# Optimization experiments

Hardware: AMD Instinct MI355X
Metric: run time of the kernel (lower is better)

## Reference

```python
import jax, jax.numpy as jnp
import numpy as np

N = 50000
IN_F = 256
HID = 32
HEADS = 4
NEG_SLOPE = 0.2


def _gat_layer(x, edge_index, W, a_src, a_dst, bias):
    # x: [N, Fin]; W: [Fin, H*C]; a_src/a_dst: [H, C]; bias: [H*C]
    n = x.shape[0]
    H, C = a_src.shape
    h = (x @ W).reshape(n, H, C)                     # [N, H, C]
    alpha_src = jnp.einsum('nhc,hc->nh', h, a_src)   # [N, H]
    alpha_dst = jnp.einsum('nhc,hc->nh', h, a_dst)   # [N, H]
    src, dst = edge_index[0], edge_index[1]
    logits = alpha_src[src] + alpha_dst[dst]         # [E, H]
    logits = jax.nn.leaky_relu(logits, negative_slope=NEG_SLOPE)
    # segment softmax over edges grouped by destination node
    seg_max = jax.ops.segment_max(logits, dst, num_segments=n)
    seg_max = jnp.where(jnp.isfinite(seg_max), seg_max, 0.0)
    e = jnp.exp(logits - seg_max[dst])               # [E, H]
    denom = jax.ops.segment_sum(e, dst, num_segments=n)  # [N, H]
    attn = e / (denom[dst] + 1e-16)                  # [E, H]
    msg = h[src] * attn[:, :, None]                  # [E, H, C]
    out = jax.ops.segment_sum(msg, dst, num_segments=n)  # [N, H, C]
    return out.reshape(n, H * C) + bias


def _add_self_loops(edge_index, n):
    # PyG GATConv default add_self_loops=True
    loops = jnp.arange(n, dtype=edge_index.dtype)
    return jnp.concatenate([edge_index, jnp.stack([loops, loops])], axis=1)


def setup_inputs() -> dict:
    key = jax.random.key(0)
    ks = jax.random.split(key, 10)
    x = jax.random.normal(ks[0], (N, IN_F), dtype=jnp.float32)
    edge_index = jax.random.randint(ks[1], (2, 800000), 0, N, dtype=jnp.int64)
    d1 = HEADS * HID
    s1 = 1.0 / np.sqrt(IN_F)
    W1 = jax.random.normal(ks[2], (IN_F, d1), dtype=jnp.float32) * s1
    a_src1 = jax.random.normal(ks[3], (HEADS, HID), dtype=jnp.float32) * 0.1
    a_dst1 = jax.random.normal(ks[4], (HEADS, HID), dtype=jnp.float32) * 0.1
    b1 = jnp.zeros((d1,), dtype=jnp.float32)
    s2 = 1.0 / np.sqrt(d1)
    W2 = jax.random.normal(ks[5], (d1, d1), dtype=jnp.float32) * s2
    a_src2 = jax.random.normal(ks[6], (HEADS, HID), dtype=jnp.float32) * 0.1
    a_dst2 = jax.random.normal(ks[7], (HEADS, HID), dtype=jnp.float32) * 0.1
    b2 = jnp.zeros((d1,), dtype=jnp.float32)
    return {"x": x, "edge_index": edge_index, "W1": W1, "a_src1": a_src1,
            "a_dst1": a_dst1, "b1": b1, "W2": W2, "a_src2": a_src2,
            "a_dst2": a_dst2, "b2": b2}


def reference(x, edge_index, W1, a_src1, a_dst1, b1, W2, a_src2, a_dst2, b2):
    # Inference mode: dropout layers are identity.
    ei = _add_self_loops(edge_index, x.shape[0])
    h = _gat_layer(x, ei, W1, a_src1, a_dst1, b1)
    h = jax.nn.elu(h)
    h = _gat_layer(h, ei, W2, a_src2, a_dst2, b2)
    return h
```

## Files before the change

### kernel.cpp

```cpp
#include <hip/hip_runtime.h>
#include <hip/hip_fp16.h>
#include <math.h>

#define HEADS 4
#define HID 32
#define D1 128
#define IN_FEAT 256
#define NEG_SLOPE 0.2f
#define CAP 64
#define AGG_NODES 4
#define NPASS 8

#define WTS_STRIDE_H 72
#define HTS_STRIDE_H 136
#define SMEM_BYTES (128 * 272)

typedef _Float16 half8 __attribute__((ext_vector_type(8)));
typedef float f32x4 __attribute__((ext_vector_type(4)));
typedef long long ll2 __attribute__((ext_vector_type(2)));

static inline int ceil_div(int a, int b) { return (a + b - 1) / b; }

static __device__ inline float2 unpack_h2(unsigned int v) {
    __half2 h = __builtin_bit_cast(__half2, v);
    return __half22float2(h);
}

__global__ void init_prep(const unsigned int* __restrict__ raw, int* __restrict__ flag,
                          const float* __restrict__ W1, _Float16* __restrict__ WT1,
                          const float* __restrict__ W2, _Float16* __restrict__ WT2) {
    int i = blockIdx.x * blockDim.x + threadIdx.x;
    if (i < IN_FEAT * D1) {
        int k = i >> 7, n = i & 127;
        WT1[(size_t)n * IN_FEAT + k] = (_Float16)W1[i];
    }
    if (i < D1 * D1) {
        int k = i >> 7, n = i & 127;
        WT2[(size_t)n * D1 + k] = (_Float16)W2[i];
    }
    if (blockIdx.x == 0 && threadIdx.x < 64) {
        unsigned int hi = raw[2 * threadIdx.x + 1];
        unsigned long long b = __ballot(hi != 0u);
        if (threadIdx.x == 0) *flag = (b == 0ULL) ? 1 : 0;
    }
}

__global__ __launch_bounds__(256) void scatter_slots(const void* __restrict__ raw,
                                                     const int* __restrict__ flag,
                                                     int* __restrict__ cnt,
                                                     unsigned short* __restrict__ slots,
                                                     int E, int N) {
    const int e0 = (blockIdx.x * blockDim.x + threadIdx.x) * 4;
    const bool wide = (*flag != 0);
    int s[4], d[4];
    bool val[4];
    if (e0 + 4 <= E) {
        if (wide) {
            const ll2* ps = (const ll2*)((const long long*)raw + e0);
            const ll2* pd = (const ll2*)((const long long*)raw + E + e0);
            ll2 a = ps[0], b = ps[1], c = pd[0], e = pd[1];
            s[0] = (int)a[0]; s[1] = (int)a[1]; s[2] = (int)b[0]; s[3] = (int)b[1];
            d[0] = (int)c[0]; d[1] = (int)c[1]; d[2] = (int)e[0]; d[3] = (int)e[1];
        } else {
            int4 a = *(const int4*)((const int*)raw + e0);
            int4 b = *(const int4*)((const int*)raw + E + e0);
            s[0] = a.x; s[1] = a.y; s[2] = a.z; s[3] = a.w;
            d[0] = b.x; d[1] = b.y; d[2] = b.z; d[3] = b.w;
        }
        val[0] = val[1] = val[2] = val[3] = true;
    } else {
#pragma unroll
        for (int i = 0; i < 4; ++i) {
            int e = e0 + i;
            val[i] = (e < E);
            if (val[i]) {
                if (wide) { s[i] = (int)((const long long*)raw)[e]; d[i] = (int)((const long long*)raw)[E + e]; }
                else      { s[i] = ((const int*)raw)[e];            d[i] = ((const int*)raw)[E + e]; }
            } else { s[i] = 0; d[i] = 0; }
        }
    }

    const int range = (N + NPASS - 1) / NPASS;
    int lo = 0;
    for (int p = 0; p < NPASS; ++p, lo += range) {
        const int hi = lo + range;
#pragma unroll
        for (int i = 0; i < 4; ++i) {
            if (val[i] && d[i] >= lo && d[i] < hi) {
                int pos = atomicAdd(&cnt[d[i]], 1);
                if (pos < CAP) slots[(size_t)d[i] * CAP + pos] = (unsigned short)s[i];
            }
        }
        __syncthreads();
    }
}

template <int AF16>
__global__ __launch_bounds__(256) void gemm128(const void* __restrict__ Ain,
                                               const _Float16* __restrict__ WT,
                                               _Float16* __restrict__ Hout,
                                               const float* __restrict__ a_src,
                                               const float* __restrict__ a_dst,
                                               float* __restrict__ asrc_out,
                                               float* __restrict__ adst_out,
                                               int M, int K) {
    __shared__ __align__(16) char smem[SMEM_BYTES];
    _Float16* WTs = (_Float16*)smem;

    const int tid = threadIdx.x;
    const int wave = tid >> 6, lane = tid & 63;
    const int quad = lane >> 4, l16 = lane & 15;
    const int row0 = blockIdx.x * 128;
    const int m0 = min(row0 + wave * 32 + l16, M - 1);
    const int m1 = min(row0 + wave * 32 + 16 + l16, M - 1);
    const float*    Af = (const float*)Ain;
    const _Float16* Ah = (const _Float16*)Ain;
    const uint4* WTg = (const uint4*)WT;
    const int K8 = K >> 3;

    f32x4 acc[2][8];
#pragma unroll
    for (int r = 0; r < 2; ++r)
#pragma unroll
        for (int c = 0; c < 8; ++c) acc[r][c] = (f32x4){0.f, 0.f, 0.f, 0.f};

    for (int kb = 0; kb < K; kb += 64) {
        __syncthreads();
#pragma unroll
        for (int i = 0; i < 4; ++i) {
            int c = tid + i * 256;
            int n = c >> 3, j = c & 7;
            uint4 v = WTg[(size_t)n * K8 + (kb >> 3) + j];
            *(uint4*)(smem + n * 144 + j * 16) = v;
        }
        __syncthreads();
#pragma unroll
        for (int kc = 0; kc < 2; ++kc) {
            int k0 = kb + kc * 32 + quad * 8;
            half8 a0f, a1f;
            if (AF16) {
                a0f = *(const half8*)(Ah + (size_t)m0 * K + k0);
                a1f = *(const half8*)(Ah + (size_t)m1 * K + k0);
            } else {
                float4 x0 = *(const float4*)(Af + (size_t)m0 * K + k0);
                float4 x1 = *(const float4*)(Af + (size_t)m0 * K + k0 + 4);
                float4 y0 = *(const float4*)(Af + (size_t)m1 * K + k0);
                float4 y1 = *(const float4*)(Af + (size_t)m1 * K + k0 + 4);
                a0f[0] = (_Float16)x0.x; a0f[1] = (_Float16)x0.y;
                a0f[2] = (_Float16)x0.z; a0f[3] = (_Float16)x0.w;
                a0f[4] = (_Float16)x1.x; a0f[5] = (_Float16)x1.y;
                a0f[6] = (_Float16)x1.z; a0f[7] = (_Float16)x1.w;
                a1f[0] = (_Float16)y0.x; a1f[1] = (_Float16)y0.y;
                a1f[2] = (_Float16)y0.z; a1f[3] = (_Float16)y0.w;
                a1f[4] = (_Float16)y1.x; a1f[5] = (_Float16)y1.y;
                a1f[6] = (_Float16)y1.z; a1f[7] = (_Float16)y1.w;
            }
#pragma unroll
            for (int c = 0; c < 8; ++c) {
                half8 bf = *(const half8*)(smem + (c * 16 + l16) * 144 + kc * 64 + quad * 16);
                acc[0][c] = __builtin_amdgcn_mfma_f32_16x16x32_f16(a0f, bf, acc[0][c], 0, 0, 0);
                acc[1][c] = __builtin_amdgcn_mfma_f32_16x16x32_f16(a1f, bf, acc[1][c], 0, 0, 0);
            }
        }
    }

    __syncthreads();
    _Float16* hts = (_Float16*)smem;
#pragma unroll
    for (int r = 0; r < 2; ++r)
#pragma unroll
        for (int c = 0; c < 8; ++c)
#pragma unroll
            for (int g = 0; g < 4; ++g) {
                int row = wave * 32 + r * 16 + quad * 4 + g;
                hts[row * HTS_STRIDE_H + c * 16 + l16] = (_Float16)acc[r][c][g];
            }
    __syncthreads();

    const int r = tid >> 1;
    const int part = tid & 1;
    const int grow = row0 + r;
    const uint4* hrow = (const uint4*)(smem + r * 272 + part * 128);
    if (grow < M) {
        uint4* dv = (uint4*)(Hout + (size_t)grow * 128 + part * 64);
#pragma unroll
        for (int i = 0; i < 8; ++i) dv[i] = hrow[i];
    }
#pragma unroll
    for (int t = 0; t < 2; ++t) {
        int hh = part * 2 + t;
        const uint4* hv = (const uint4*)(smem + r * 272 + hh * 64);
        const float4* as4 = (const float4*)(a_src + hh * HID);
        const float4* ad4 = (const float4*)(a_dst + hh * HID);
        float ps = 0.f, pd = 0.f;
#pragma unroll
        for (int b = 0; b < 4; ++b) {
            uint4 u = hv[b];
            float2 f0 = unpack_h2(u.x), f1 = unpack_h2(u.y);
            float2 f2 = unpack_h2(u.z), f3 = unpack_h2(u.w);
            float4 s0 = as4[b * 2], s1 = as4[b * 2 + 1];
            float4 d0 = ad4[b * 2], d1 = ad4[b * 2 + 1];
            ps += f0.x * s0.x + f0.y * s0.y + f1.x * s0.z + f1.y * s0.w
                + f2.x * s1.x + f2.y * s1.y + f3.x * s1.z + f3.y * s1.w;
            pd += f0.x * d0.x + f0.y * d0.y + f1.x * d0.z + f1.y * d0.w
                + f2.x * d1.x + f2.y * d1.y + f3.x * d1.z + f3.y * d1.w;
        }
        if (grow < M) {
            asrc_out[grow * 4 + hh] = ps;
            adst_out[grow * 4 + hh] = pd;
        }
    }
}

__global__ __launch_bounds__(256) void aggregate(const _Float16* __restrict__ hb,
                                                 const int* __restrict__ cnt,
                                                 const unsigned short* __restrict__ slots,
                                                 const float* __restrict__ asrc,
                                                 const float* __restrict__ adst,
                                                 const float* __restrict__ bias,
                                                 float* __restrict__ out32,
                                                 _Float16* __restrict__ out16,
                                                 int N, int apply_elu) {
    const int w = threadIdx.x >> 6;
    const int lane = threadIdx.x & 63;
    const int node = blockIdx.x * AGG_NODES + w;
    const bool live = (node < N);

    __shared__ float wsh[AGG_NODES][CAP][4];
    __shared__ int ssh[AGG_NODES][CAP];

    int cntE = 0, count = 1;
    if (live) {
        cntE = min(cnt[node], CAP - 1);
        count = cntE + 1;
    }
    const unsigned short* nslots = slots + (size_t)node * CAP;

    float4 ad4 = live ? *(const float4*)&adst[node * 4] : make_float4(0.f, 0.f, 0.f, 0.f);

    float lv[4] = {-1e30f, -1e30f, -1e30f, -1e30f};
    if (live && lane < count) {
        int src = (lane < cntE) ? (int)nslots[lane] : node;
        ssh[w][lane] = src;
        float4 as4 = *(const float4*)&asrc[src * 4];
        float t0 = as4.x + ad4.x, t1 = as4.y + ad4.y;
        float t2 = as4.z + ad4.z, t3 = as4.w + ad4.w;
        lv[0] = t0 > 0.f ? t0 : NEG_SLOPE * t0;
        lv[1] = t1 > 0.f ? t1 : NEG_SLOPE * t1;
        lv[2] = t2 > 0.f ? t2 : NEG_SLOPE * t2;
        lv[3] = t3 > 0.f ? t3 : NEG_SLOPE * t3;
    }
    float m[4] = {lv[0], lv[1], lv[2], lv[3]};
#pragma unroll
    for (int off = 32; off >= 1; off >>= 1)
#pragma unroll
        for (int h = 0; h < 4; ++h)
            m[h] = fmaxf(m[h], __shfl_xor(m[h], off, 64));
    float ex[4], sum[4];
#pragma unroll
    for (int h = 0; h < 4; ++h) {
        ex[h] = (lane < count) ? __expf(lv[h] - m[h]) : 0.f;
        sum[h] = ex[h];
    }
#pragma unroll
    for (int off = 32; off >= 1; off >>= 1)
#pragma unroll
        for (int h = 0; h < 4; ++h)
            sum[h] += __shfl_xor(sum[h], off, 64);
    if (live && lane < count) {
        float4 w4;
        w4.x = ex[0] / (sum[0] + 1e-16f);
        w4.y = ex[1] / (sum[1] + 1e-16f);
        w4.z = ex[2] / (sum[2] + 1e-16f);
        w4.w = ex[3] / (sum[3] + 1e-16f);
        *(float4*)&wsh[w][lane][0] = w4;
    }
    __syncthreads();

    const int quarter = lane >> 4;
    const int sub = lane & 15;
    const int hh = sub >> 2;
    const unsigned int* hw = (const unsigned int*)hb;

    float acc[8];
#pragma unroll
    for (int i = 0; i < 8; ++i) acc[i] = 0.f;

    if (live) {
        int j = quarter;
        if (j + 4 < count) {
            int s0 = ssh[w][j], s1 = ssh[w][j + 4];
            float w0 = wsh[w][j][hh], w1 = wsh[w][j + 4][hh];
            uint4 u0 = *(const uint4*)(hw + (size_t)s0 * 64 + sub * 4);
            uint4 u1 = *(const uint4*)(hw + (size_t)s1 * 64 + sub * 4);
            for (j += 8; j + 4 < count; j += 8) {
                int t0 = ssh[w][j], t1 = ssh[w][j + 4];
                float x0 = wsh[w][j][hh], x1 = wsh[w][j + 4][hh];
                uint4 v0 = *(const uint4*)(hw + (size_t)t0 * 64 + sub * 4);
                uint4 v1 = *(const uint4*)(hw + (size_t)t1 * 64 + sub * 4);
                const __half2* p0 = (const __half2*)&u0;
                const __half2* p1 = (const __half2*)&u1;
#pragma unroll
                for (int q = 0; q < 4; ++q) {
                    acc[2 * q + 0] = fmaf((float)__low2half(p0[q]),  w0, acc[2 * q + 0]);
                    acc[2 * q + 1] = fmaf((float)__high2half(p0[q]), w0, acc[2 * q + 1]);
                }
#pragma unroll
                for (int q = 0; q < 4; ++q) {
                    acc[2 * q + 0] = fmaf((float)__low2half(p1[q]),  w1, acc[2 * q + 0]);
                    acc[2 * q + 1] = fmaf((float)__high2half(p1[q]), w1, acc[2 * q + 1]);
                }
                u0 = v0; u1 = v1; w0 = x0; w1 = x1;
            }
            {
                const __half2* p0 = (const __half2*)&u0;
                const __half2* p1 = (const __half2*)&u1;
#pragma unroll
                for (int q = 0; q < 4; ++q) {
                    acc[2 * q + 0] = fmaf((float)__low2half(p0[q]),  w0, acc[2 * q + 0]);
                    acc[2 * q + 1] = fmaf((float)__high2half(p0[q]), w0, acc[2 * q + 1]);
                }
#pragma unroll
                for (int q = 0; q < 4; ++q) {
                    acc[2 * q + 0] = fmaf((float)__low2half(p1[q]),  w1, acc[2 * q + 0]);
                    acc[2 * q + 1] = fmaf((float)__high2half(p1[q]), w1, acc[2 * q + 1]);
                }
            }
        }
        if (j < count) {
            int s0 = ssh[w][j];
            float w0 = wsh[w][j][hh];
            uint4 u0 = *(const uint4*)(hw + (size_t)s0 * 64 + sub * 4);
            const __half2* p0 = (const __half2*)&u0;
#pragma unroll
            for (int q = 0; q < 4; ++q) {
                acc[2 * q + 0] = fmaf((float)__low2half(p0[q]),  w0, acc[2 * q + 0]);
                acc[2 * q + 1] = fmaf((float)__high2half(p0[q]), w0, acc[2 * q + 1]);
            }
        }
    }

#pragma unroll
    for (int i = 0; i < 8; ++i) {
        acc[i] += __shfl_xor(acc[i], 16, 64);
        acc[i] += __shfl_xor(acc[i], 32, 64);
    }

    if (live && quarter == 0) {
        int ch8 = sub * 8;
        float o[8];
#pragma unroll
        for (int i = 0; i < 8; ++i) o[i] = acc[i] + bias[ch8 + i];
        if (apply_elu) {
#pragma unroll
            for (int i = 0; i < 8; ++i) o[i] = o[i] > 0.f ? o[i] : __expf(o[i]) - 1.f;
        }
        if (out16) {
            __align__(16) _Float16 t[8];
#pragma unroll
            for (int i = 0; i < 8; ++i) t[i] = (_Float16)o[i];
            *(uint4*)&out16[(size_t)node * D1 + ch8] = *(const uint4*)t;
        } else {
            *(float4*)&out32[(size_t)node * D1 + ch8]     = make_float4(o[0], o[1], o[2], o[3]);
            *(float4*)&out32[(size_t)node * D1 + ch8 + 4] = make_float4(o[4], o[5], o[6], o[7]);
        }
    }
}

extern "C" void kernel_launch(void* const* d_in, const int* in_sizes, int n_in,
                              void* d_out, int out_size, void* d_ws, size_t ws_size,
                              hipStream_t stream) {
    const float* x      = (const float*)d_in[0];
    const void*  e_raw  = d_in[1];
    const float* W1     = (const float*)d_in[2];
    const float* a_src1 = (const float*)d_in[3];
    const float* a_dst1 = (const float*)d_in[4];
    const float* b1     = (const float*)d_in[5];
    const float* W2     = (const float*)d_in[6];
    const float* a_src2 = (const float*)d_in[7];
    const float* a_dst2 = (const float*)d_in[8];
    const float* b2     = (const float*)d_in[9];

    const int N  = in_sizes[0] / IN_FEAT;
    const int E  = in_sizes[1] / 2;
    float* out = (float*)d_out;

    char* ws = (char*)d_ws;
    size_t woff = 0;
    auto walloc = [&](size_t bytes) -> char* {
        char* p = ws + woff;
        woff = (woff + bytes + 255) & ~(size_t)255;
        return p;
    };
    int*   flag  = (int*)walloc(4);
    int*   cnt   = (int*)walloc((size_t)N * 4);
    unsigned short* slots = (unsigned short*)walloc((size_t)N * CAP * 2);
    float* asrc  = (float*)walloc((size_t)N * HEADS * 4);
    float* adst  = (float*)walloc((size_t)N * HEADS * 4);
    _Float16* hb  = (_Float16*)walloc((size_t)N * D1 * 2);
    _Float16* o16 = (_Float16*)walloc((size_t)N * D1 * 2);
    _Float16* WT1 = (_Float16*)walloc((size_t)IN_FEAT * D1 * 2);
    _Float16* WT2 = (_Float16*)walloc((size_t)D1 * D1 * 2);

    const int Gg = ceil_div(N, 128);
    const int Ga = ceil_div(N, AGG_NODES);

    hipMemsetAsync(cnt, 0, (size_t)N * 4, stream);
    init_prep<<<ceil_div(IN_FEAT * D1, 256), 256, 0, stream>>>(
        (const unsigned int*)e_raw, flag, W1, WT1, W2, WT2);
    scatter_slots<<<ceil_div(E, 1024), 256, 0, stream>>>(e_raw, flag, cnt, slots, E, N);
    gemm128<0><<<Gg, 256, 0, stream>>>(x, WT1, hb, a_src1, a_dst1, asrc, adst, N, IN_FEAT);
    aggregate<<<Ga, 256, 0, stream>>>(hb, cnt, slots, asrc, adst, b1, nullptr, o16, N, 1);
    gemm128<1><<<Gg, 256, 0, stream>>>(o16, WT2, hb, a_src2, a_dst2, asrc, adst, N, D1);
    aggregate<<<Ga, 256, 0, stream>>>(hb, cnt, slots, asrc, adst, b2, out, nullptr, N, 0);
}
```

Measured before the change: 273.0 us.

## Merge edge scatter into first GEMM launch and double edges per thread

The edge-slot scatter kernel and the first-layer GEMM are combined into one launch. The first Sg blocks do the scatter and the remaining blocks do the GEMM, so the two independent stages can overlap on the GPU and one launch is saved. Each scatter thread now handles 8 edges instead of 4, which halves the scatter block count. Scatter blocks now also reserve the GEMM's shared-memory allocation, which may lower their occupancy.

```diff
diff --git a/kernel.cpp b/kernel.cpp
--- a/kernel.cpp
+++ b/kernel.cpp
@@ -10,6 +10,7 @@
 #define CAP 64
 #define AGG_NODES 4
 #define NPASS 8
+#define EPT 8
 
 #define WTS_STRIDE_H 72
 #define HTS_STRIDE_H 136
@@ -45,32 +46,40 @@
     }
 }
 
-__global__ __launch_bounds__(256) void scatter_slots(const void* __restrict__ raw,
-                                                     const int* __restrict__ flag,
-                                                     int* __restrict__ cnt,
-                                                     unsigned short* __restrict__ slots,
-                                                     int E, int N) {
-    const int e0 = (blockIdx.x * blockDim.x + threadIdx.x) * 4;
+__device__ void scatter_body(int sbid, const void* __restrict__ raw,
+                             const int* __restrict__ flag,
+                             int* __restrict__ cnt,
+                             unsigned short* __restrict__ slots,
+                             int E, int N) {
+    const int e0 = (sbid * 256 + (int)threadIdx.x) * EPT;
     const bool wide = (*flag != 0);
-    int s[4], d[4];
-    bool val[4];
-    if (e0 + 4 <= E) {
+    int s[EPT], d[EPT];
+    bool val[EPT];
+    if (e0 + EPT <= E) {
         if (wide) {
             const ll2* ps = (const ll2*)((const long long*)raw + e0);
             const ll2* pd = (const ll2*)((const long long*)raw + E + e0);
-            ll2 a = ps[0], b = ps[1], c = pd[0], e = pd[1];
-            s[0] = (int)a[0]; s[1] = (int)a[1]; s[2] = (int)b[0]; s[3] = (int)b[1];
-            d[0] = (int)c[0]; d[1] = (int)c[1]; d[2] = (int)e[0]; d[3] = (int)e[1];
+#pragma unroll
+            for (int i = 0; i < EPT / 2; ++i) {
+                ll2 a = ps[i], b = pd[i];
+                s[2 * i] = (int)a[0]; s[2 * i + 1] = (int)a[1];
+                d[2 * i] = (int)b[0]; d[2 * i + 1] = (int)b[1];
+            }
         } else {
-            int4 a = *(const int4*)((const int*)raw + e0);
-            int4 b = *(const int4*)((const int*)raw + E + e0);
-            s[0] = a.x; s[1] = a.y; s[2] = a.z; s[3] = a.w;
-            d[0] = b.x; d[1] = b.y; d[2] = b.z; d[3] = b.w;
-        }
-        val[0] = val[1] = val[2] = val[3] = true;
+            const int4* ps = (const int4*)((const int*)raw + e0);
+            const int4* pd = (const int4*)((const int*)raw + E + e0);
+#pragma unroll
+            for (int i = 0; i < EPT / 4; ++i) {
+                int4 a = ps[i], b = pd[i];
+                s[4 * i] = a.x; s[4 * i + 1] = a.y; s[4 * i + 2] = a.z; s[4 * i + 3] = a.w;
+                d[4 * i] = b.x; d[4 * i + 1] = b.y; d[4 * i + 2] = b.z; d[4 * i + 3] = b.w;
+            }
+        }
+#pragma unroll
+        for (int i = 0; i < EPT; ++i) val[i] = true;
     } else {
 #pragma unroll
-        for (int i = 0; i < 4; ++i) {
+        for (int i = 0; i < EPT; ++i) {
             int e = e0 + i;
             val[i] = (e < E);
             if (val[i]) {
@@ -85,7 +94,7 @@
     for (int p = 0; p < NPASS; ++p, lo += range) {
         const int hi = lo + range;
 #pragma unroll
-        for (int i = 0; i < 4; ++i) {
+        for (int i = 0; i < EPT; ++i) {
             if (val[i] && d[i] >= lo && d[i] < hi) {
                 int pos = atomicAdd(&cnt[d[i]], 1);
                 if (pos < CAP) slots[(size_t)d[i] * CAP + pos] = (unsigned short)s[i];
@@ -96,21 +105,18 @@
 }
 
 template <int AF16>
-__global__ __launch_bounds__(256) void gemm128(const void* __restrict__ Ain,
-                                               const _Float16* __restrict__ WT,
-                                               _Float16* __restrict__ Hout,
-                                               const float* __restrict__ a_src,
-                                               const float* __restrict__ a_dst,
-                                               float* __restrict__ asrc_out,
-                                               float* __restrict__ adst_out,
-                                               int M, int K) {
-    __shared__ __align__(16) char smem[SMEM_BYTES];
-    _Float16* WTs = (_Float16*)smem;
-
+__device__ void gemm_body(char* smem, int bid, const void* __restrict__ Ain,
+                          const _Float16* __restrict__ WT,
+                          _Float16* __restrict__ Hout,
+                          const float* __restrict__ a_src,
+                          const float* __restrict__ a_dst,
+                          float* __restrict__ asrc_out,
+                          float* __restrict__ adst_out,
+                          int M, int K) {
     const int tid = threadIdx.x;
     const int wave = tid >> 6, lane = tid & 63;
     const int quad = lane >> 4, l16 = lane & 15;
-    const int row0 = blockIdx.x * 128;
+    const int row0 = bid * 128;
     const int m0 = min(row0 + wave * 32 + l16, M - 1);
     const int m1 = min(row0 + wave * 32 + 16 + l16, M - 1);
     const float*    Af = (const float*)Ain;
@@ -212,6 +218,43 @@
     }
 }
 
+template <int AF16>
+__global__ __launch_bounds__(256) void gemm128(const void* __restrict__ Ain,
+                                               const _Float16* __restrict__ WT,
+                                               _Float16* __restrict__ Hout,
+                                               const float* __restrict__ a_src,
+                                               const float* __restrict__ a_dst,
+                                               float* __restrict__ asrc_out,
+                                               float* __restrict__ adst_out,
+                                               int M, int K) {
+    __shared__ __align__(16) char smem[SMEM_BYTES];
+    gemm_body<AF16>(smem, blockIdx.x, Ain, WT, Hout, a_src, a_dst,
+                    asrc_out, adst_out, M, K);
+}
+
+template <int AF16>
+__global__ __launch_bounds__(256) void gemm128_scatter(const void* __restrict__ Ain,
+                                                       const _Float16* __restrict__ WT,
+                                                       _Float16* __restrict__ Hout,
+                                                       const float* __restrict__ a_src,
+                                                       const float* __restrict__ a_dst,
+                                                       float* __restrict__ asrc_out,
+                                                       float* __restrict__ adst_out,
+                                                       int M, int K,
+                                                       const void* __restrict__ raw,
+                                                       const int* __restrict__ flag,
+                                                       int* __restrict__ cnt,
+                                                       unsigned short* __restrict__ slots,
+                                                       int E, int Sg) {
+    __shared__ __align__(16) char smem[SMEM_BYTES];
+    if ((int)blockIdx.x < Sg) {
+        scatter_body(blockIdx.x, raw, flag, cnt, slots, E, M);
+        return;
+    }
+    gemm_body<AF16>(smem, blockIdx.x - Sg, Ain, WT, Hout, a_src, a_dst,
+                    asrc_out, adst_out, M, K);
+}
+
 __global__ __launch_bounds__(256) void aggregate(const _Float16* __restrict__ hb,
                                                  const int* __restrict__ cnt,
                                                  const unsigned short* __restrict__ slots,
@@ -403,13 +446,15 @@
     _Float16* WT2 = (_Float16*)walloc((size_t)D1 * D1 * 2);
 
     const int Gg = ceil_div(N, 128);
+    const int Sg = ceil_div(E, 256 * EPT);
     const int Ga = ceil_div(N, AGG_NODES);
 
     hipMemsetAsync(cnt, 0, (size_t)N * 4, stream);
     init_prep<<<ceil_div(IN_FEAT * D1, 256), 256, 0, stream>>>(
         (const unsigned int*)e_raw, flag, W1, WT1, W2, WT2);
-    scatter_slots<<<ceil_div(E, 1024), 256, 0, stream>>>(e_raw, flag, cnt, slots, E, N);
-    gemm128<0><<<Gg, 256, 0, stream>>>(x, WT1, hb, a_src1, a_dst1, asrc, adst, N, IN_FEAT);
+    gemm128_scatter<0><<<Sg + Gg, 256, 0, stream>>>(
+        x, WT1, hb, a_src1, a_dst1, asrc, adst, N, IN_FEAT,
+        e_raw, flag, cnt, slots, E, Sg);
     aggregate<<<Ga, 256, 0, stream>>>(hb, cnt, slots, asrc, adst, b1, nullptr, o16, N, 1);
     gemm128<1><<<Gg, 256, 0, stream>>>(o16, WT2, hb, a_src2, a_dst2, asrc, adst, N, D1);
     aggregate<<<Ga, 256, 0, stream>>>(hb, cnt, slots, asrc, adst, b2, out, nullptr, N, 0);
```

Measured after the change: 265.5 us. 1.03x faster.
